# Kernel tuning notes

Hardware: AMD Instinct MI355X
Metric: run time of the kernel (lower is better)

## Reference

```python
import jax, jax.numpy as jnp
import numpy as np
import math

B, S, D, H = 2, 2048, 1024, 16
DK = D // H


def setup_inputs() -> dict:
    key = jax.random.key(0)
    ks = jax.random.split(key, 11)
    f = jnp.float32
    return {
        "query": jax.random.normal(ks[0], (B, S, D), f),
        "key": jax.random.normal(ks[1], (B, S, D), f),
        "value": jax.random.normal(ks[2], (B, S, D), f),
        "wq": jax.random.normal(ks[3], (D, D), f) * 0.02,
        "bq": jnp.zeros((D,), f),
        "wk": jax.random.normal(ks[4], (D, D), f) * 0.02,
        "bk": jnp.zeros((D,), f),
        "wv": jax.random.normal(ks[5], (D, D), f) * 0.02,
        "bv": jnp.zeros((D,), f),
        "wo": jax.random.normal(ks[6], (D, D), f) * 0.02,
        "bo": jnp.zeros((D,), f),
    }


def reference(query, key, value, wq, bq, wk, bk, wv, bv, wo, bo):
    # Linear projections (torch Linear: y = x @ W.T + b)
    q = query @ wq.T + bq
    k = key @ wk.T + bk
    v = value @ wv.T + bv
    # [B,S,D] -> [B,H,S,DK]
    q = q.reshape(B, S, H, DK).transpose(0, 2, 1, 3)
    k = k.reshape(B, S, H, DK).transpose(0, 2, 1, 3)
    v = v.reshape(B, S, H, DK).transpose(0, 2, 1, 3)
    scores = jnp.einsum("bhqd,bhkd->bhqk", q, k) / math.sqrt(DK)
    causal = jnp.triu(jnp.ones((S, S), dtype=bool), k=1)  # strict upper triangle masked
    scores = jnp.where(causal, -jnp.inf, scores)
    attn = jax.nn.softmax(scores, axis=-1)  # dropout is identity in eval (p=0)
    x = jnp.einsum("bhqk,bhkd->bhqd", attn, v)
    x = x.transpose(0, 2, 1, 3).reshape(B, S, D)
    return x @ wo.T + bo
```

## Files before the change

### kernel.cpp

```cpp
#include <hip/hip_runtime.h>
#include <math.h>

#define BB 2
#define SS 2048
#define DD 1024
#define HH 16
#define DKK 64
#define MM (BB * SS)
#define KK DD
#define VSTR 2176

typedef __attribute__((ext_vector_type(8))) short short8;
typedef __attribute__((ext_vector_type(4))) float floatx4;

__device__ inline unsigned short f2bf(float x) {
    unsigned int u = __float_as_uint(x);
    u += 0x7fffu + ((u >> 16) & 1u);
    return (unsigned short)(u >> 16);
}

__device__ inline unsigned int pkbf(float a, float b) {
    return (__float_as_uint(b) & 0xffff0000u) | (__float_as_uint(a) >> 16);
}

__device__ inline void cast4f(const float* __restrict__ in, unsigned short* __restrict__ out, int i) {
    const float4 v = *(const float4*)(in + i);
    unsigned long long pk = (unsigned long long)f2bf(v.x)
                          | ((unsigned long long)f2bf(v.y) << 16)
                          | ((unsigned long long)f2bf(v.z) << 32)
                          | ((unsigned long long)f2bf(v.w) << 48);
    *(unsigned long long*)(out + i) = pk;
}

__global__ __launch_bounds__(256) void cast_all(const float* __restrict__ q, const float* __restrict__ k,
                                                const float* __restrict__ v,
                                                const float* __restrict__ wq, const float* __restrict__ wk,
                                                const float* __restrict__ wv, const float* __restrict__ wo,
                                                unsigned short* __restrict__ oq, unsigned short* __restrict__ ok,
                                                unsigned short* __restrict__ ov,
                                                unsigned short* __restrict__ owq, unsigned short* __restrict__ owk,
                                                unsigned short* __restrict__ owv, unsigned short* __restrict__ owo) {
    const int blk = blockIdx.x;
    const float* in;
    unsigned short* out;
    int idx;
    if (blk < 12288) {
        const int w = blk >> 12;
        idx = blk & 4095;
        in  = (w == 0) ? q : (w == 1) ? k : v;
        out = (w == 0) ? oq : (w == 1) ? ok : ov;
    } else {
        const int w = (blk - 12288) >> 10;
        idx = (blk - 12288) & 1023;
        in  = (w == 0) ? wq : (w == 1) ? wk : (w == 2) ? wv : wo;
        out = (w == 0) ? owq : (w == 1) ? owk : (w == 2) ? owv : owo;
    }
    cast4f(in, out, (idx * 256 + threadIdx.x) * 4);
}

#define GLDS(gp, lp) __builtin_amdgcn_global_load_lds( \
    (const __attribute__((address_space(1))) void*)(gp), \
    (__attribute__((address_space(3))) void*)(lp), 16, 0, 0)

__device__ __forceinline__ void gemm_body(const unsigned short* __restrict__ A,
                                          const unsigned short* __restrict__ W,
                                          const float* __restrict__ bias,
                                          void* __restrict__ Cout, int mode, int blk,
                                          unsigned short* As, unsigned short* Bs) {
    const int t    = threadIdx.x;
    const int lane = t & 63;
    const int wave = t >> 6;
    const int col  = lane & 15;
    const int quad = lane >> 4;

    const int m0  = (blk & 63) * 64;
    const int n0  = (blk >> 6) * 128;
    const int wm0 = (wave & 1) * 32;
    const int wn0 = (wave >> 1) * 64;

    const int sw = ((t & 3) ^ ((t >> 3) & 3)) * 8;
    const size_t arow = (size_t)(m0 + (t >> 2)) * KK + sw;
    const size_t brow = (size_t)(n0 + (t >> 2)) * KK + sw;
    const int rseg = (quad ^ ((col >> 1) & 3)) * 8;

    floatx4 acc[2][4] = {};

    GLDS(A + arow,           &As[(t >> 2) * 32 + sw]);
    GLDS(W + brow,           &Bs[(t >> 2) * 32 + sw]);
    GLDS(W + brow + 64 * KK, &Bs[(64 + (t >> 2)) * 32 + sw]);

    int cur = 0;
    for (int kb = 0; kb < KK / 32; ++kb) {
        __syncthreads();

        if (kb + 1 < KK / 32) {
            const int k0 = (kb + 1) * 32;
            const int nx = cur ^ 1;
            GLDS(A + arow + k0,           &As[nx * 64 * 32 + (t >> 2) * 32 + sw]);
            GLDS(W + brow + k0,           &Bs[nx * 128 * 32 + (t >> 2) * 32 + sw]);
            GLDS(W + brow + k0 + 64 * KK, &Bs[nx * 128 * 32 + (64 + (t >> 2)) * 32 + sw]);
        }

        const unsigned short* Ab = &As[cur * 64 * 32];
        const unsigned short* Bb = &Bs[cur * 128 * 32];
        short8 a[2], b[4];
        #pragma unroll
        for (int i = 0; i < 2; ++i)
            a[i] = *(const short8*)(Ab + (wm0 + i * 16 + col) * 32 + rseg);
        #pragma unroll
        for (int j = 0; j < 4; ++j)
            b[j] = *(const short8*)(Bb + (wn0 + j * 16 + col) * 32 + rseg);

        #pragma unroll
        for (int i = 0; i < 2; ++i)
            #pragma unroll
            for (int j = 0; j < 4; ++j)
                acc[i][j] = __builtin_amdgcn_mfma_f32_16x16x32_bf16(a[i], b[j], acc[i][j], 0, 0, 0);

        cur ^= 1;
    }

    #pragma unroll
    for (int i = 0; i < 2; ++i) {
        #pragma unroll
        for (int j = 0; j < 4; ++j) {
            const int n  = n0 + wn0 + j * 16 + col;
            const float bv = bias[n];
            #pragma unroll
            for (int r = 0; r < 4; ++r) {
                const int m = m0 + wm0 + i * 16 + quad * 4 + r;
                const float v = acc[i][j][r] + bv;
                ((float*)Cout)[(size_t)m * DD + n] = v;
            }
        }
    }
    (void)mode;
}

__global__ __launch_bounds__(256) void gemm_qkv(const unsigned short* __restrict__ qB,
                                                const unsigned short* __restrict__ kB,
                                                const unsigned short* __restrict__ vB,
                                                const unsigned short* __restrict__ wqB,
                                                const unsigned short* __restrict__ wkB,
                                                const unsigned short* __restrict__ wvB,
                                                const float* __restrict__ bq,
                                                const float* __restrict__ bk,
                                                const float* __restrict__ bv,
                                                unsigned short* __restrict__ Qh,
                                                unsigned short* __restrict__ Kh,
                                                unsigned short* __restrict__ Vt) {
    __shared__ __align__(16) unsigned short As[2 * 128 * 32];
    __shared__ __align__(16) unsigned short Bs[2 * 128 * 32];

    const int which = blockIdx.x >> 8;
    const int blk   = blockIdx.x & 255;
    const unsigned short* A = (which == 0) ? qB : (which == 1) ? kB : vB;
    const unsigned short* W = (which == 0) ? wqB : (which == 1) ? wkB : wvB;
    const float* bias       = (which == 0) ? bq : (which == 1) ? bk : bv;

    const int t    = threadIdx.x;
    const int lane = t & 63;
    const int wave = t >> 6;
    const int col  = lane & 15;
    const int quad = lane >> 4;

    const int m0  = (blk & 31) * 128;
    const int n0  = (blk >> 5) * 128;
    const int wm0 = (wave & 1) * 64;
    const int wn0 = (wave >> 1) * 64;

    const int sw = ((t & 3) ^ ((t >> 3) & 3)) * 8;
    const size_t arow = (size_t)(m0 + (t >> 2)) * KK + sw;
    const size_t brow = (size_t)(n0 + (t >> 2)) * KK + sw;
    const int rseg = (quad ^ ((col >> 1) & 3)) * 8;

    floatx4 acc[4][4] = {};

    GLDS(A + arow,           &As[(t >> 2) * 32 + sw]);
    GLDS(A + arow + 64 * KK, &As[(64 + (t >> 2)) * 32 + sw]);
    GLDS(W + brow,           &Bs[(t >> 2) * 32 + sw]);
    GLDS(W + brow + 64 * KK, &Bs[(64 + (t >> 2)) * 32 + sw]);

    int cur = 0;
    for (int kb = 0; kb < KK / 32; ++kb) {
        __syncthreads();

        if (kb + 1 < KK / 32) {
            const int k0 = (kb + 1) * 32;
            const int nx = cur ^ 1;
            GLDS(A + arow + k0,           &As[nx * 128 * 32 + (t >> 2) * 32 + sw]);
            GLDS(A + arow + k0 + 64 * KK, &As[nx * 128 * 32 + (64 + (t >> 2)) * 32 + sw]);
            GLDS(W + brow + k0,           &Bs[nx * 128 * 32 + (t >> 2) * 32 + sw]);
            GLDS(W + brow + k0 + 64 * KK, &Bs[nx * 128 * 32 + (64 + (t >> 2)) * 32 + sw]);
        }

        const unsigned short* Ab = &As[cur * 128 * 32];
        const unsigned short* Bb = &Bs[cur * 128 * 32];
        short8 a[4], b[4];
        #pragma unroll
        for (int i = 0; i < 4; ++i)
            a[i] = *(const short8*)(Ab + (wm0 + i * 16 + col) * 32 + rseg);
        #pragma unroll
        for (int j = 0; j < 4; ++j)
            b[j] = *(const short8*)(Bb + (wn0 + j * 16 + col) * 32 + rseg);

        #pragma unroll
        for (int i = 0; i < 4; ++i)
            #pragma unroll
            for (int j = 0; j < 4; ++j)
                acc[i][j] = __builtin_amdgcn_mfma_f32_16x16x32_bf16(a[i], b[j], acc[i][j], 0, 0, 0);

        cur ^= 1;
    }

    #pragma unroll
    for (int i = 0; i < 4; ++i) {
        #pragma unroll
        for (int j = 0; j < 4; ++j) {
            const int n  = n0 + wn0 + j * 16 + col;
            const float bv = bias[n];
            const int h = n / DKK, dk = n % DKK;
            #pragma unroll
            for (int r = 0; r < 4; ++r) {
                const int m = m0 + wm0 + i * 16 + quad * 4 + r;
                const int bdx = m / SS, s = m % SS;
                const float v = acc[i][j][r] + bv;
                if (which != 2) {
                    unsigned short* O = (which == 0) ? Qh : Kh;
                    O[(((size_t)(bdx * HH + h)) * SS + s) * DKK + dk] = f2bf(v);
                } else {
                    Vt[(((size_t)(bdx * HH + h)) * DKK + dk) * VSTR + s] = f2bf(v);
                }
            }
        }
    }
}

__global__ __launch_bounds__(256) void gemm_out(const unsigned short* __restrict__ A,
                                                const unsigned short* __restrict__ W,
                                                const float* __restrict__ bias,
                                                float* __restrict__ C) {
    __shared__ __align__(16) unsigned short As[2 * 64 * 32];
    __shared__ __align__(16) unsigned short Bs[2 * 128 * 32];
    gemm_body(A, W, bias, C, 2, blockIdx.x, As, Bs);
}

#define C1 0.18033688011112042f
#define C2 11.541560327111707f
#define MFMA __builtin_amdgcn_mfma_f32_16x16x32_bf16

__global__ __launch_bounds__(256) void attn_mfma(const unsigned short* __restrict__ Qh,
                                                 const unsigned short* __restrict__ Kh,
                                                 const unsigned short* __restrict__ Vt,
                                                 unsigned short* __restrict__ X) {
    __shared__ __align__(16) unsigned short Ks[2][64 * 64];
    __shared__ __align__(16) unsigned short Vs[2][64 * 64];
    __shared__ __align__(16) unsigned short Plds[4][16 * 40];

    const int t    = threadIdx.x;
    const int lane = t & 63;
    const int wave = t >> 6;
    const int col  = lane & 15;
    const int quad = lane >> 4;

    const int lin = blockIdx.x;
    const int bh  = (lin & 7) + 8 * ((lin >> 3) & 3);
    const int c   = 31 - (lin >> 5);
    const int b   = bh / HH, h = bh % HH;

    const unsigned short* Kb = Kh + (size_t)bh * SS * DKK;
    const unsigned short* Vb = Vt + (size_t)bh * DKK * VSTR;

    const int r0  = t >> 3;
    const int r1  = (t + 256) >> 3;
    const int sg0 = ((t & 7) ^ (r0 & 7)) * 8;
    const int sg1 = ((t & 7) ^ (r1 & 7)) * 8;

    const int q0 = c * 64 + wave * 16;
    unsigned short* Pw = &Plds[wave][0];

    const unsigned short* Qb = Qh + ((size_t)bh * SS + q0) * DKK;
    const short8 qa0 = *(const short8*)(Qb + (size_t)col * DKK + quad * 8);
    const short8 qa1 = *(const short8*)(Qb + (size_t)col * DKK + 32 + quad * 8);

    floatx4 o0 = {0.f, 0.f, 0.f, 0.f}, o1 = o0, o2 = o0, o3 = o0;
    float lp = 0.f;

    const int nst = c + 1;

    const int ksA = ((quad)      ^ (col & 7)) * 8;
    const int ksB = ((quad | 4)  ^ (col & 7)) * 8;

    GLDS(Kb + (size_t)r0 * DKK + sg0,  &Ks[0][t * 8]);
    GLDS(Kb + (size_t)r1 * DKK + sg1,  &Ks[0][(t + 256) * 8]);
    GLDS(Vb + (size_t)r0 * VSTR + sg0, &Vs[0][t * 8]);
    GLDS(Vb + (size_t)r1 * VSTR + sg1, &Vs[0][(t + 256) * 8]);

    int cur = 0;
    for (int kb = 0; kb < nst; ++kb) {
        __syncthreads();

        if (kb + 1 < nst) {
            const int jn = (kb + 1) * 64;
            const int nx = cur ^ 1;
            GLDS(Kb + (size_t)(jn + r0) * DKK + sg0,  &Ks[nx][t * 8]);
            GLDS(Kb + (size_t)(jn + r1) * DKK + sg1,  &Ks[nx][(t + 256) * 8]);
            GLDS(Vb + (size_t)r0 * VSTR + jn + sg0,   &Vs[nx][t * 8]);
            GLDS(Vb + (size_t)r1 * VSTR + jn + sg1,   &Vs[nx][(t + 256) * 8]);
        }

        const unsigned short* Kp = &Ks[cur][0];
        const unsigned short* Vp = &Vs[cur][0];

        #pragma unroll
        for (int hh = 0; hh < 2; ++hh) {
            const int j0 = kb * 64 + hh * 32;
            if (j0 < q0 + 16) {
                const short8 k0 = *(const short8*)(Kp + (hh * 32 + col) * 64 + ksA);
                const short8 k1 = *(const short8*)(Kp + (hh * 32 + col) * 64 + ksB);
                const short8 k2 = *(const short8*)(Kp + (hh * 32 + col + 16) * 64 + ksA);
                const short8 k3 = *(const short8*)(Kp + (hh * 32 + col + 16) * 64 + ksB);

                floatx4 t0 = {0.f, 0.f, 0.f, 0.f}, t1 = t0;
                t0 = MFMA(k0, qa0, t0, 0, 0, 0);
                t0 = MFMA(k1, qa1, t0, 0, 0, 0);
                t1 = MFMA(k2, qa0, t1, 0, 0, 0);
                t1 = MFMA(k3, qa1, t1, 0, 0, 0);

                float p[8];
                if (j0 + 31 > q0) {
                    const int lim = q0 + col - j0;
                    #pragma unroll
                    for (int r = 0; r < 4; ++r) {
                        p[r]     = (quad * 4 + r      <= lim) ? __builtin_exp2f(fmaf(t0[r], C1, -C2)) : 0.f;
                        p[4 + r] = (16 + quad * 4 + r <= lim) ? __builtin_exp2f(fmaf(t1[r], C1, -C2)) : 0.f;
                    }
                } else {
                    #pragma unroll
                    for (int r = 0; r < 4; ++r) {
                        p[r]     = __builtin_exp2f(fmaf(t0[r], C1, -C2));
                        p[4 + r] = __builtin_exp2f(fmaf(t1[r], C1, -C2));
                    }
                }
                lp += (p[0] + p[1]) + (p[2] + p[3]) + (p[4] + p[5]) + (p[6] + p[7]);

                uint2 w0 = { pkbf(p[0], p[1]), pkbf(p[2], p[3]) };
                uint2 w1 = { pkbf(p[4], p[5]), pkbf(p[6], p[7]) };
                *(uint2*)(Pw + col * 40 + quad * 4)      = w0;
                *(uint2*)(Pw + col * 40 + 16 + quad * 4) = w1;

                const short8 pb = *(const short8*)(Pw + col * 40 + quad * 8);
                const int vs = hh ? ksB : ksA;
                const short8 v0 = *(const short8*)(Vp + (col)      * 64 + vs);
                const short8 v1 = *(const short8*)(Vp + (col + 16) * 64 + vs);
                const short8 v2 = *(const short8*)(Vp + (col + 32) * 64 + vs);
                const short8 v3 = *(const short8*)(Vp + (col + 48) * 64 + vs);
                o0 = MFMA(v0, pb, o0, 0, 0, 0);
                o1 = MFMA(v1, pb, o1, 0, 0, 0);
                o2 = MFMA(v2, pb, o2, 0, 0, 0);
                o3 = MFMA(v3, pb, o3, 0, 0, 0);
            }
        }

        cur ^= 1;
    }

    lp += __shfl_xor(lp, 16, 64);
    lp += __shfl_xor(lp, 32, 64);
    const float li = 1.f / lp;

    unsigned short* Xp = X + ((size_t)(b * SS + q0 + col)) * DD + h * DKK + quad * 4;
    {
        uint2 w;
        w.x = (unsigned int)f2bf(o0[0] * li) | ((unsigned int)f2bf(o0[1] * li) << 16);
        w.y = (unsigned int)f2bf(o0[2] * li) | ((unsigned int)f2bf(o0[3] * li) << 16);
        *(uint2*)(Xp + 0) = w;
        w.x = (unsigned int)f2bf(o1[0] * li) | ((unsigned int)f2bf(o1[1] * li) << 16);
        w.y = (unsigned int)f2bf(o1[2] * li) | ((unsigned int)f2bf(o1[3] * li) << 16);
        *(uint2*)(Xp + 16) = w;
        w.x = (unsigned int)f2bf(o2[0] * li) | ((unsigned int)f2bf(o2[1] * li) << 16);
        w.y = (unsigned int)f2bf(o2[2] * li) | ((unsigned int)f2bf(o2[3] * li) << 16);
        *(uint2*)(Xp + 32) = w;
        w.x = (unsigned int)f2bf(o3[0] * li) | ((unsigned int)f2bf(o3[1] * li) << 16);
        w.y = (unsigned int)f2bf(o3[2] * li) | ((unsigned int)f2bf(o3[3] * li) << 16);
        *(uint2*)(Xp + 48) = w;
    }
}

extern "C" void kernel_launch(void* const* d_in, const int* in_sizes, int n_in,
                              void* d_out, int out_size, void* d_ws, size_t ws_size,
                              hipStream_t stream) {
    const float* query = (const float*)d_in[0];
    const float* key   = (const float*)d_in[1];
    const float* value = (const float*)d_in[2];
    const float* wq    = (const float*)d_in[3];
    const float* bq    = (const float*)d_in[4];
    const float* wk    = (const float*)d_in[5];
    const float* bk    = (const float*)d_in[6];
    const float* wv    = (const float*)d_in[7];
    const float* bv    = (const float*)d_in[8];
    const float* wo    = (const float*)d_in[9];
    const float* bo    = (const float*)d_in[10];

    char* ws = (char*)d_ws;
    const size_t MB = 1024 * 1024;
    unsigned short* qB  = (unsigned short*)(ws);
    unsigned short* kB  = (unsigned short*)(ws + 8 * MB);
    unsigned short* vB  = (unsigned short*)(ws + 16 * MB);
    unsigned short* wqB = (unsigned short*)(ws + 24 * MB);
    unsigned short* wkB = (unsigned short*)(ws + 26 * MB);
    unsigned short* wvB = (unsigned short*)(ws + 28 * MB);
    unsigned short* woB = (unsigned short*)(ws + 30 * MB);
    unsigned short* Qh  = (unsigned short*)(ws + 32 * MB);
    unsigned short* Kh  = (unsigned short*)(ws + 40 * MB);
    unsigned short* Vt  = (unsigned short*)(ws + 48 * MB);
    unsigned short* Xb  = qB;

    cast_all<<<16384, 256, 0, stream>>>(query, key, value, wq, wk, wv, wo,
                                        qB, kB, vB, wqB, wkB, wvB, woB);

    gemm_qkv<<<768, 256, 0, stream>>>(qB, kB, vB, wqB, wkB, wvB, bq, bk, bv, Qh, Kh, Vt);

    attn_mfma<<<1024, 256, 0, stream>>>(Qh, Kh, Vt, Xb);

    gemm_out<<<512, 256, 0, stream>>>(Xb, woB, bo, (float*)d_out);
}
```

Measured before the change: 229.5 us.

## Rewrite QKV and output GEMMs with larger tiles and explicit pipelining

Replaces both projection GEMMs with a shared templated mainloop that uses 256x256 (QKV) and 128x256 (output) tiles, 512-thread blocks, and a K-step of 64 with a two-deep global-to-LDS prefetch. Barriers, vmcnt waits and sched barriers are placed by hand so MFMA work overlaps the next tile's loads, s_setprio raises priority during the second half of the MFMAs, and block IDs are remapped across the 8 XCDs to improve L2 locality. The V-transpose store is packed into 8-byte writes. The larger tiles cut the grids to 192 and 128 blocks, which may underfill a 256-CU device.

```diff
diff --git a/kernel.cpp b/kernel.cpp
--- a/kernel.cpp
+++ b/kernel.cpp
@@ -62,187 +62,198 @@
     (const __attribute__((address_space(1))) void*)(gp), \
     (__attribute__((address_space(3))) void*)(lp), 16, 0, 0)
 
-__device__ __forceinline__ void gemm_body(const unsigned short* __restrict__ A,
-                                          const unsigned short* __restrict__ W,
-                                          const float* __restrict__ bias,
-                                          void* __restrict__ Cout, int mode, int blk,
-                                          unsigned short* As, unsigned short* Bs) {
+#define SCHED0() __builtin_amdgcn_sched_barrier(0)
+#define BAR()    __builtin_amdgcn_s_barrier()
+#define WAITL0() asm volatile("s_waitcnt lgkmcnt(0)" ::: "memory")
+#define WAITV(n) asm volatile("s_waitcnt vmcnt(" #n ")" ::: "memory")
+
+template<int MT>
+__device__ __forceinline__ void gemm_mainloop(const unsigned short* __restrict__ A,
+                                              const unsigned short* __restrict__ W,
+                                              int m0, int n0,
+                                              unsigned short* __restrict__ As,
+                                              unsigned short* __restrict__ Bs,
+                                              floatx4 (&acc)[MT * 4][4]) {
     const int t    = threadIdx.x;
     const int lane = t & 63;
     const int wave = t >> 6;
     const int col  = lane & 15;
     const int quad = lane >> 4;
-
-    const int m0  = (blk & 63) * 64;
-    const int n0  = (blk >> 6) * 128;
-    const int wm0 = (wave & 1) * 32;
-    const int wn0 = (wave >> 1) * 64;
-
-    const int sw = ((t & 3) ^ ((t >> 3) & 3)) * 8;
-    const size_t arow = (size_t)(m0 + (t >> 2)) * KK + sw;
-    const size_t brow = (size_t)(n0 + (t >> 2)) * KK + sw;
-    const int rseg = (quad ^ ((col >> 1) & 3)) * 8;
-
-    floatx4 acc[2][4] = {};
-
-    GLDS(A + arow,           &As[(t >> 2) * 32 + sw]);
-    GLDS(W + brow,           &Bs[(t >> 2) * 32 + sw]);
-    GLDS(W + brow + 64 * KK, &Bs[(64 + (t >> 2)) * 32 + sw]);
-
-    int cur = 0;
-    for (int kb = 0; kb < KK / 32; ++kb) {
-        __syncthreads();
-
-        if (kb + 1 < KK / 32) {
-            const int k0 = (kb + 1) * 32;
-            const int nx = cur ^ 1;
-            GLDS(A + arow + k0,           &As[nx * 64 * 32 + (t >> 2) * 32 + sw]);
-            GLDS(W + brow + k0,           &Bs[nx * 128 * 32 + (t >> 2) * 32 + sw]);
-            GLDS(W + brow + k0 + 64 * KK, &Bs[nx * 128 * 32 + (64 + (t >> 2)) * 32 + sw]);
-        }
-
-        const unsigned short* Ab = &As[cur * 64 * 32];
-        const unsigned short* Bb = &Bs[cur * 128 * 32];
-        short8 a[2], b[4];
-        #pragma unroll
-        for (int i = 0; i < 2; ++i)
-            a[i] = *(const short8*)(Ab + (wm0 + i * 16 + col) * 32 + rseg);
-        #pragma unroll
-        for (int j = 0; j < 4; ++j)
-            b[j] = *(const short8*)(Bb + (wn0 + j * 16 + col) * 32 + rseg);
-
-        #pragma unroll
-        for (int i = 0; i < 2; ++i)
+    const int wr   = wave >> 2;
+    const int wc   = wave & 3;
+    const int wm   = wr * (MT * 64);
+    const int wn   = wc * 64;
+
+    const int r   = t >> 3;
+    const int cs  = t & 7;
+    const int ksw = (cs ^ (r & 7)) * 8;
+
+    const int sA0 = (quad ^ (col & 7)) * 8;
+    const int sA1 = ((quad + 4) ^ (col & 7)) * 8;
+
+    auto stage = [&](int kt, int pb) {
+        const int k0 = kt * 64;
+        #pragma unroll
+        for (int g = 0; g < 2 * MT; ++g)
+            GLDS(A + (size_t)(m0 + g * 64 + r) * KK + k0 + ksw,
+                 &As[pb * (MT * 128 * 64) + (g * 64 + r) * 64 + cs * 8]);
+        #pragma unroll
+        for (int g = 0; g < 4; ++g)
+            GLDS(W + (size_t)(n0 + g * 64 + r) * KK + k0 + ksw,
+                 &Bs[pb * (256 * 64) + (g * 64 + r) * 64 + cs * 8]);
+    };
+
+    stage(0, 0);
+    stage(1, 1);
+    if constexpr (MT == 2) { WAITV(8); } else { WAITV(6); }
+    SCHED0(); BAR(); SCHED0();
+
+    const int NK = KK / 64;
+    for (int kt = 0; kt < NK; ++kt) {
+        const int p = kt & 1;
+        const unsigned short* Ab = &As[p * (MT * 128 * 64)];
+        const unsigned short* Bb = &Bs[p * (256 * 64)];
+
+        short8 a0[MT * 4], a1[MT * 4], b0[4], b1[4];
+        #pragma unroll
+        for (int i = 0; i < MT * 4; ++i) {
+            const unsigned short* ar = Ab + (wm + i * 16 + col) * 64;
+            a0[i] = *(const short8*)(ar + sA0);
+            a1[i] = *(const short8*)(ar + sA1);
+        }
+        #pragma unroll
+        for (int j = 0; j < 4; ++j) {
+            const unsigned short* br = Bb + (wn + j * 16 + col) * 64;
+            b0[j] = *(const short8*)(br + sA0);
+            b1[j] = *(const short8*)(br + sA1);
+        }
+
+        #pragma unroll
+        for (int i = 0; i < MT * 4; ++i)
             #pragma unroll
             for (int j = 0; j < 4; ++j)
-                acc[i][j] = __builtin_amdgcn_mfma_f32_16x16x32_bf16(a[i], b[j], acc[i][j], 0, 0, 0);
-
-        cur ^= 1;
-    }
-
-    #pragma unroll
-    for (int i = 0; i < 2; ++i) {
-        #pragma unroll
-        for (int j = 0; j < 4; ++j) {
-            const int n  = n0 + wn0 + j * 16 + col;
-            const float bv = bias[n];
+                acc[i][j] = __builtin_amdgcn_mfma_f32_16x16x32_bf16(a0[i], b0[j], acc[i][j], 0, 0, 0);
+
+        WAITL0(); SCHED0();
+        BAR(); SCHED0();
+
+        if (kt + 2 < NK) stage(kt + 2, p);
+
+        __builtin_amdgcn_s_setprio(1);
+        #pragma unroll
+        for (int i = 0; i < MT * 4; ++i)
             #pragma unroll
-            for (int r = 0; r < 4; ++r) {
-                const int m = m0 + wm0 + i * 16 + quad * 4 + r;
-                const float v = acc[i][j][r] + bv;
-                ((float*)Cout)[(size_t)m * DD + n] = v;
-            }
-        }
-    }
-    (void)mode;
-}
-
-__global__ __launch_bounds__(256) void gemm_qkv(const unsigned short* __restrict__ qB,
-                                                const unsigned short* __restrict__ kB,
-                                                const unsigned short* __restrict__ vB,
-                                                const unsigned short* __restrict__ wqB,
-                                                const unsigned short* __restrict__ wkB,
-                                                const unsigned short* __restrict__ wvB,
-                                                const float* __restrict__ bq,
-                                                const float* __restrict__ bk,
-                                                const float* __restrict__ bv,
-                                                unsigned short* __restrict__ Qh,
-                                                unsigned short* __restrict__ Kh,
-                                                unsigned short* __restrict__ Vt) {
-    __shared__ __align__(16) unsigned short As[2 * 128 * 32];
-    __shared__ __align__(16) unsigned short Bs[2 * 128 * 32];
-
-    const int which = blockIdx.x >> 8;
-    const int blk   = blockIdx.x & 255;
+            for (int j = 0; j < 4; ++j)
+                acc[i][j] = __builtin_amdgcn_mfma_f32_16x16x32_bf16(a1[i], b1[j], acc[i][j], 0, 0, 0);
+        __builtin_amdgcn_s_setprio(0);
+
+        if (kt + 2 < NK) {
+            if constexpr (MT == 2) { WAITV(8); } else { WAITV(6); }
+        } else {
+            WAITV(0);
+        }
+        SCHED0(); BAR(); SCHED0();
+    }
+}
+
+__global__ __launch_bounds__(512, 2) void gemm_qkv(const unsigned short* __restrict__ qB,
+                                                   const unsigned short* __restrict__ kB,
+                                                   const unsigned short* __restrict__ vB,
+                                                   const unsigned short* __restrict__ wqB,
+                                                   const unsigned short* __restrict__ wkB,
+                                                   const unsigned short* __restrict__ wvB,
+                                                   const float* __restrict__ bq,
+                                                   const float* __restrict__ bk,
+                                                   const float* __restrict__ bv,
+                                                   unsigned short* __restrict__ Qh,
+                                                   unsigned short* __restrict__ Kh,
+                                                   unsigned short* __restrict__ Vt) {
+    __shared__ __align__(16) unsigned short As[2 * 256 * 64];
+    __shared__ __align__(16) unsigned short Bs[2 * 256 * 64];
+
+    const int bid   = blockIdx.x;
+    const int wgid  = (bid & 7) * 24 + (bid >> 3);
+    const int which = wgid >> 6;
+    const int tile  = wgid & 63;
+    const int m0    = (tile & 15) * 256;
+    const int n0    = (tile >> 4) * 256;
+
     const unsigned short* A = (which == 0) ? qB : (which == 1) ? kB : vB;
     const unsigned short* W = (which == 0) ? wqB : (which == 1) ? wkB : wvB;
     const float* bias       = (which == 0) ? bq : (which == 1) ? bk : bv;
+
+    floatx4 acc[8][4] = {};
+    gemm_mainloop<2>(A, W, m0, n0, As, Bs, acc);
 
     const int t    = threadIdx.x;
     const int lane = t & 63;
     const int wave = t >> 6;
     const int col  = lane & 15;
     const int quad = lane >> 4;
-
-    const int m0  = (blk & 31) * 128;
-    const int n0  = (blk >> 5) * 128;
-    const int wm0 = (wave & 1) * 64;
-    const int wn0 = (wave >> 1) * 64;
-
-    const int sw = ((t & 3) ^ ((t >> 3) & 3)) * 8;
-    const size_t arow = (size_t)(m0 + (t >> 2)) * KK + sw;
-    const size_t brow = (size_t)(n0 + (t >> 2)) * KK + sw;
-    const int rseg = (quad ^ ((col >> 1) & 3)) * 8;
+    const int wm   = (wave >> 2) * 128;
+    const int wn   = (wave & 3) * 64;
+
+    #pragma unroll
+    for (int i = 0; i < 8; ++i) {
+        #pragma unroll
+        for (int j = 0; j < 4; ++j) {
+            const int n  = n0 + wn + j * 16 + col;
+            const float bv0 = bias[n];
+            const int h = n >> 6, dk = n & 63;
+            const int mb  = m0 + wm + i * 16 + quad * 4;
+            const int bdx = mb >> 11, s = mb & 2047;
+            if (which != 2) {
+                unsigned short* O = (which == 0) ? Qh : Kh;
+                #pragma unroll
+                for (int rr = 0; rr < 4; ++rr)
+                    O[(((size_t)(bdx * HH + h)) * SS + (s + rr)) * DKK + dk] = f2bf(acc[i][j][rr] + bv0);
+            } else {
+                unsigned short* vp = Vt + (((size_t)(bdx * HH + h)) * DKK + dk) * VSTR + s;
+                uint2 w;
+                w.x = (unsigned int)f2bf(acc[i][j][0] + bv0) | ((unsigned int)f2bf(acc[i][j][1] + bv0) << 16);
+                w.y = (unsigned int)f2bf(acc[i][j][2] + bv0) | ((unsigned int)f2bf(acc[i][j][3] + bv0) << 16);
+                *(uint2*)vp = w;
+            }
+        }
+    }
+}
+
+__global__ __launch_bounds__(512, 2) void gemm_out(const unsigned short* __restrict__ A,
+                                                   const unsigned short* __restrict__ W,
+                                                   const float* __restrict__ bias,
+                                                   float* __restrict__ C) {
+    __shared__ __align__(16) unsigned short As[2 * 128 * 64];
+    __shared__ __align__(16) unsigned short Bs[2 * 256 * 64];
+
+    const int bid  = blockIdx.x;
+    const int wgid = (bid & 7) * 16 + (bid >> 3);
+    const int m0   = (wgid & 31) * 128;
+    const int n0   = (wgid >> 5) * 256;
 
     floatx4 acc[4][4] = {};
-
-    GLDS(A + arow,           &As[(t >> 2) * 32 + sw]);
-    GLDS(A + arow + 64 * KK, &As[(64 + (t >> 2)) * 32 + sw]);
-    GLDS(W + brow,           &Bs[(t >> 2) * 32 + sw]);
-    GLDS(W + brow + 64 * KK, &Bs[(64 + (t >> 2)) * 32 + sw]);
-
-    int cur = 0;
-    for (int kb = 0; kb < KK / 32; ++kb) {
-        __syncthreads();
-
-        if (kb + 1 < KK / 32) {
-            const int k0 = (kb + 1) * 32;
-            const int nx = cur ^ 1;
-            GLDS(A + arow + k0,           &As[nx * 128 * 32 + (t >> 2) * 32 + sw]);
-            GLDS(A + arow + k0 + 64 * KK, &As[nx * 128 * 32 + (64 + (t >> 2)) * 32 + sw]);
-            GLDS(W + brow + k0,           &Bs[nx * 128 * 32 + (t >> 2) * 32 + sw]);
-            GLDS(W + brow + k0 + 64 * KK, &Bs[nx * 128 * 32 + (64 + (t >> 2)) * 32 + sw]);
-        }
-
-        const unsigned short* Ab = &As[cur * 128 * 32];
-        const unsigned short* Bb = &Bs[cur * 128 * 32];
-        short8 a[4], b[4];
-        #pragma unroll
-        for (int i = 0; i < 4; ++i)
-            a[i] = *(const short8*)(Ab + (wm0 + i * 16 + col) * 32 + rseg);
-        #pragma unroll
-        for (int j = 0; j < 4; ++j)
-            b[j] = *(const short8*)(Bb + (wn0 + j * 16 + col) * 32 + rseg);
-
-        #pragma unroll
-        for (int i = 0; i < 4; ++i)
-            #pragma unroll
-            for (int j = 0; j < 4; ++j)
-                acc[i][j] = __builtin_amdgcn_mfma_f32_16x16x32_bf16(a[i], b[j], acc[i][j], 0, 0, 0);
-
-        cur ^= 1;
-    }
+    gemm_mainloop<1>(A, W, m0, n0, As, Bs, acc);
+
+    const int t    = threadIdx.x;
+    const int lane = t & 63;
+    const int wave = t >> 6;
+    const int col  = lane & 15;
+    const int quad = lane >> 4;
+    const int wm   = (wave >> 2) * 64;
+    const int wn   = (wave & 3) * 64;
 
     #pragma unroll
     for (int i = 0; i < 4; ++i) {
         #pragma unroll
         for (int j = 0; j < 4; ++j) {
-            const int n  = n0 + wn0 + j * 16 + col;
-            const float bv = bias[n];
-            const int h = n / DKK, dk = n % DKK;
+            const int n = n0 + wn + j * 16 + col;
+            const float bv0 = bias[n];
             #pragma unroll
-            for (int r = 0; r < 4; ++r) {
-                const int m = m0 + wm0 + i * 16 + quad * 4 + r;
-                const int bdx = m / SS, s = m % SS;
-                const float v = acc[i][j][r] + bv;
-                if (which != 2) {
-                    unsigned short* O = (which == 0) ? Qh : Kh;
-                    O[(((size_t)(bdx * HH + h)) * SS + s) * DKK + dk] = f2bf(v);
-                } else {
-                    Vt[(((size_t)(bdx * HH + h)) * DKK + dk) * VSTR + s] = f2bf(v);
-                }
+            for (int rr = 0; rr < 4; ++rr) {
+                const int m = m0 + wm + i * 16 + quad * 4 + rr;
+                C[(size_t)m * DD + n] = acc[i][j][rr] + bv0;
             }
         }
     }
-}
-
-__global__ __launch_bounds__(256) void gemm_out(const unsigned short* __restrict__ A,
-                                                const unsigned short* __restrict__ W,
-                                                const float* __restrict__ bias,
-                                                float* __restrict__ C) {
-    __shared__ __align__(16) unsigned short As[2 * 64 * 32];
-    __shared__ __align__(16) unsigned short Bs[2 * 128 * 32];
-    gemm_body(A, W, bias, C, 2, blockIdx.x, As, Bs);
 }
 
 #define C1 0.18033688011112042f
@@ -419,9 +430,9 @@
     cast_all<<<16384, 256, 0, stream>>>(query, key, value, wq, wk, wv, wo,
                                         qB, kB, vB, wqB, wkB, wvB, woB);
 
-    gemm_qkv<<<768, 256, 0, stream>>>(qB, kB, vB, wqB, wkB, wvB, bq, bk, bv, Qh, Kh, Vt);
+    gemm_qkv<<<192, 512, 0, stream>>>(qB, kB, vB, wqB, wkB, wvB, bq, bk, bv, Qh, Kh, Vt);
 
     attn_mfma<<<1024, 256, 0, stream>>>(Qh, Kh, Vt, Xb);
 
-    gemm_out<<<512, 256, 0, stream>>>(Xb, woB, bo, (float*)d_out);
-}
+    gemm_out<<<128, 512, 0, stream>>>(Xb, woB, bo, (float*)d_out);
+}
```

Result: faster. 218.3 us (-4.9%).
